# Optimization experiments

Measured on AMD Instinct MI355X. Metric: run time of the kernel, lower is better.

Reference implementation:

```python
import jax, jax.numpy as jnp
import numpy as np
import math

HEAD_DIM = 128
N_HEADS = 32
N_KV_HEADS = 8
ROPE_THETA = 10000.0


def _rotate_half(x):
    x1, x2 = jnp.split(x, 2, axis=-1)
    return jnp.concatenate([-x2, x1], axis=-1)


def _rope_cos_sin(position_ids, head_dim, theta):
    # position_ids: [B, S] int
    inv_freq = 1.0 / (theta ** (jnp.arange(0, head_dim, 2, dtype=jnp.float32) / head_dim))
    freqs = position_ids.astype(jnp.float32)[..., None] * inv_freq[None, None, :]  # [B,S,D/2]
    emb = jnp.concatenate([freqs, freqs], axis=-1)  # [B,S,D]
    return jnp.cos(emb), jnp.sin(emb)


def setup_inputs() -> dict:
    key = jax.random.key(0)
    k1, k2, k3, k4, k5 = jax.random.split(key, 5)
    B, S, H = 1, 2048, 4096
    hidden_states = jax.random.normal(k1, (B, S, H), dtype=jnp.float32)
    Wq = jax.random.normal(k2, (N_HEADS * HEAD_DIM, H), dtype=jnp.float32) * (1.0 / math.sqrt(H))
    Wk = jax.random.normal(k3, (N_KV_HEADS * HEAD_DIM, H), dtype=jnp.float32) * (1.0 / math.sqrt(H))
    Wv = jax.random.normal(k4, (N_KV_HEADS * HEAD_DIM, H), dtype=jnp.float32) * (1.0 / math.sqrt(H))
    Wo = jax.random.normal(k5, (H, N_HEADS * HEAD_DIM), dtype=jnp.float32) * (1.0 / math.sqrt(H))
    position_ids = jnp.arange(S, dtype=jnp.int32)[None, :]
    return {"hidden_states": hidden_states, "Wq": Wq, "Wk": Wk, "Wv": Wv, "Wo": Wo,
            "position_ids": position_ids}


def reference(hidden_states, Wq, Wk, Wv, Wo, position_ids):
    B, S, H = hidden_states.shape
    d = HEAD_DIM
    groups = N_HEADS // N_KV_HEADS

    # projections (torch Linear: x @ W^T)
    q = (hidden_states @ Wq.T).reshape(B, S, N_HEADS, d).transpose(0, 2, 1, 3)      # [B,Hq,S,d]
    k = (hidden_states @ Wk.T).reshape(B, S, N_KV_HEADS, d).transpose(0, 2, 1, 3)   # [B,Hk,S,d]
    v = (hidden_states @ Wv.T).reshape(B, S, N_KV_HEADS, d).transpose(0, 2, 1, 3)

    cos, sin = _rope_cos_sin(position_ids, d, ROPE_THETA)  # [B,S,d]
    cos = cos[:, None, :, :]
    sin = sin[:, None, :, :]
    q = q * cos + _rotate_half(q) * sin
    k = k * cos + _rotate_half(k) * sin

    # GQA: repeat kv heads
    k = jnp.repeat(k, groups, axis=1)  # [B,Hq,S,d]
    v = jnp.repeat(v, groups, axis=1)

    scores = jnp.einsum('bhqd,bhkd->bhqk', q, k) / math.sqrt(d)
    causal = jnp.tril(jnp.ones((S, S), dtype=bool))
    scores = jnp.where(causal[None, None], scores, jnp.finfo(jnp.float32).min)
    attn = jax.nn.softmax(scores.astype(jnp.float32), axis=-1).astype(q.dtype)

    out = jnp.einsum('bhqk,bhkd->bhqd', attn, v)        # [B,Hq,S,d]
    out = out.transpose(0, 2, 1, 3).reshape(B, S, N_HEADS * d)
    return out @ Wo.T
```

## Files before the change

kernel.cpp:

```cpp
#include <hip/hip_runtime.h>
#include <hip/hip_bf16.h>
#include <cstdint>
#include <cstddef>

#define S_LEN 2048
#define HID   4096
#define HD    128
#define NH    32
#define NKV   8
#define KVW   (NKV * HD)
#define QKVN  (HID + 2 * KVW)

typedef __bf16 bf16x8_t __attribute__((ext_vector_type(8)));
typedef float  f32x4_t  __attribute__((ext_vector_type(4)));
typedef unsigned short u16x8_t __attribute__((ext_vector_type(8)));

__device__ __forceinline__ unsigned short f2b(float f) {
  unsigned u = __float_as_uint(f);
  u += 0x7FFFu + ((u >> 16) & 1u);
  return (unsigned short)(u >> 16);
}
__device__ __forceinline__ float b2f(unsigned short v) {
  return __uint_as_float(((unsigned)v) << 16);
}
__device__ __forceinline__ void gld_lds16(const void* g, void* l) {
  __builtin_amdgcn_global_load_lds(
      (const __attribute__((address_space(1))) void*)g,
      (__attribute__((address_space(3))) void*)l, 16, 0, 0);
}

__global__ void cvt_kernel(const float* __restrict__ src,
                           unsigned short* __restrict__ dst, int n4) {
  int i = blockIdx.x * blockDim.x + threadIdx.x;
  int stride = gridDim.x * blockDim.x;
  for (; i < n4; i += stride) {
    float4 v = reinterpret_cast<const float4*>(src)[i];
    ushort4 o;
    o.x = f2b(v.x); o.y = f2b(v.y); o.z = f2b(v.z); o.w = f2b(v.w);
    reinterpret_cast<ushort4*>(dst)[i] = o;
  }
}

__global__ void rope_kernel(unsigned short* __restrict__ Q,
                            unsigned short* __restrict__ Kb,
                            const int* __restrict__ pos_ids) {
  const int total = S_LEN * (NH + NKV) * 64;
  int idx = blockIdx.x * blockDim.x + threadIdx.x;
  int stride = gridDim.x * blockDim.x;
  for (; idx < total; idx += stride) {
    int s   = idx / ((NH + NKV) * 64);
    int rem = idx % ((NH + NKV) * 64);
    int hp  = rem >> 6;
    int i   = rem & 63;
    unsigned short* ptr; int W, h;
    if (hp < NH) { ptr = Q;  W = HID; h = hp; }
    else         { ptr = Kb; W = KVW; h = hp - NH; }
    float pos = (float)pos_ids[s];
    float ang = pos * __expf(-(float)i * 0.14391156516f);
    float sn, cs;
    sincosf(ang, &sn, &cs);
    size_t base = (size_t)s * W + (size_t)h * HD + i;
    float lo = b2f(ptr[base]);
    float hi = b2f(ptr[base + 64]);
    ptr[base]      = f2b(lo * cs - hi * sn);
    ptr[base + 64] = f2b(hi * cs + lo * sn);
  }
}

template <int BN, int MODE>
__global__ __launch_bounds__(512, 2) void gemm8p_kernel(
    const unsigned short* __restrict__ A, const unsigned short* __restrict__ B,
    void* __restrict__ C0, void* __restrict__ C1, void* __restrict__ C2,
    int N, int K) {
  constexpr int NFR = BN / 64;
  constexpr int ABYTES = 256 * 128;
  constexpr int TILE_LDS = ABYTES + BN * 128;
  constexpr int VM_N = NFR + 2;
  __shared__ char ldsB[2 * TILE_LDS];

  const int tid  = threadIdx.x;
  const int lane = tid & 63;
  const int wid  = tid >> 6;
  const int wm = wid >> 2, wn = wid & 3;
  const int lr = lane & 15, g = lane >> 4;
  const int bm = blockIdx.y * 256;
  const int bn = blockIdx.x * BN;
  const int nk = K >> 6;
  const int ni = nk >> 1;
  const int xr = (lr & 7) << 4;

  auto stage_u = [&](int t, int u) {
    if (t >= nk) return;
    const int riu = tid >> 3;
    const int cbs = ((tid & 7) << 4) ^ ((riu & 7) << 4);
    const char* src;
    if (u < 4)
      src = (const char*)A + ((size_t)(bm + u * 64 + riu) * K + t * 64) * 2 + cbs;
    else
      src = (const char*)B + ((size_t)(bn + (u - 4) * 64 + riu) * K + t * 64) * 2 + cbs;
    gld_lds16(src, ldsB + (t & 1) * TILE_LDS + u * 8192 + tid * 16);
  };

  auto rdA = [&](const char* bb, int m, int k) {
    const int row = wm * 128 + m * 16 + lr;
    return *(const bf16x8_t*)(bb + row * 128 + ((k * 64 + g * 16) ^ xr));
  };
  auto rdB = [&](const char* bb, int n, int k) {
    const int row = wn * (BN / 4) + n * 16 + lr;
    return *(const bf16x8_t*)(bb + ABYTES + row * 128 + ((k * 64 + g * 16) ^ xr));
  };

  for (int t = 0; t < 2; ++t)
    for (int u = 0; u < 4 + NFR; ++u) stage_u(t, u);
  asm volatile("s_waitcnt vmcnt(0)" ::: "memory");
  __builtin_amdgcn_sched_barrier(0);
  __builtin_amdgcn_s_barrier();

  f32x4_t acc[8][NFR];
#pragma unroll
  for (int m = 0; m < 8; ++m)
#pragma unroll
    for (int n = 0; n < NFR; ++n) acc[m][n] = f32x4_t{0.f, 0.f, 0.f, 0.f};

  bf16x8_t bfr[NFR][2], af[2][2];

#define MFMA_BLOCK(MB)                                                        \
  __builtin_amdgcn_s_setprio(1);                                              \
  _Pragma("unroll") for (int m = 0; m < 2; ++m)                               \
    _Pragma("unroll") for (int n = 0; n < NFR; ++n)                           \
      _Pragma("unroll") for (int k = 0; k < 2; ++k)                           \
        acc[(MB) + m][n] = __builtin_amdgcn_mfma_f32_16x16x32_bf16(           \
            af[m][k], bfr[n][k], acc[(MB) + m][n], 0, 0, 0);                  \
  __builtin_amdgcn_s_setprio(0);

#define GATE()                                                                \
  __builtin_amdgcn_s_barrier();                                               \
  asm volatile("s_waitcnt lgkmcnt(0)" ::: "memory");                          \
  __builtin_amdgcn_sched_barrier(0);

#define RD_A2(bb, m0)                                                         \
  _Pragma("unroll") for (int m = 0; m < 2; ++m)                               \
    _Pragma("unroll") for (int k = 0; k < 2; ++k)                             \
      af[m][k] = rdA(bb, (m0) + m, k);

  for (int i = 0; i < ni; ++i) {
    const char* baseE = ldsB;
    const char* baseO = ldsB + TILE_LDS;
    const int tO = 2 * i + 1, tE2 = 2 * i + 2, tO2 = 2 * i + 3;
    const bool last = (i == ni - 1);

#pragma unroll
    for (int n = 0; n < NFR; ++n)
#pragma unroll
      for (int k = 0; k < 2; ++k) bfr[n][k] = rdB(baseE, n, k);
    RD_A2(baseE, 0);
    if (i > 0) { stage_u(tO, 1); stage_u(tO, 3); }
    GATE(); MFMA_BLOCK(0);
    __builtin_amdgcn_s_barrier();

    RD_A2(baseE, 2);
    stage_u(tE2, 4); stage_u(tE2, 5);
    GATE(); MFMA_BLOCK(2);
    __builtin_amdgcn_s_barrier();

    RD_A2(baseE, 4);
    if constexpr (NFR == 3) { stage_u(tE2, 6); stage_u(tE2, 0); }
    else                    { stage_u(tE2, 0); stage_u(tE2, 2); }
    GATE(); MFMA_BLOCK(4);
    __builtin_amdgcn_s_barrier();

    RD_A2(baseE, 6);
    if constexpr (NFR == 3) { stage_u(tE2, 2); }
    GATE(); MFMA_BLOCK(6);
    if (last) { asm volatile("s_waitcnt vmcnt(0)" ::: "memory"); }
    else      { asm volatile("s_waitcnt vmcnt(%0)" :: "n"(VM_N) : "memory"); }
    __builtin_amdgcn_sched_barrier(0);
    __builtin_amdgcn_s_barrier();

#pragma unroll
    for (int n = 0; n < NFR; ++n)
#pragma unroll
      for (int k = 0; k < 2; ++k) bfr[n][k] = rdB(baseO, n, k);
    RD_A2(baseO, 0);
    stage_u(tE2, 1); stage_u(tE2, 3);
    GATE(); MFMA_BLOCK(0);
    __builtin_amdgcn_s_barrier();

    RD_A2(baseO, 2);
    stage_u(tO2, 4); stage_u(tO2, 5);
    GATE(); MFMA_BLOCK(2);
    __builtin_amdgcn_s_barrier();

    RD_A2(baseO, 4);
    if constexpr (NFR == 3) { stage_u(tO2, 6); stage_u(tO2, 0); }
    else                    { stage_u(tO2, 0); stage_u(tO2, 2); }
    GATE(); MFMA_BLOCK(4);
    __builtin_amdgcn_s_barrier();

    RD_A2(baseO, 6);
    if constexpr (NFR == 3) { stage_u(tO2, 2); }
    GATE(); MFMA_BLOCK(6);
    if (!last) { asm volatile("s_waitcnt vmcnt(%0)" :: "n"(VM_N) : "memory"); }
    __builtin_amdgcn_sched_barrier(0);
    __builtin_amdgcn_s_barrier();
  }
#undef MFMA_BLOCK
#undef GATE
#undef RD_A2

#pragma unroll
  for (int mf = 0; mf < 8; ++mf) {
    const int row0 = bm + wm * 128 + mf * 16 + g * 4;
#pragma unroll
    for (int nf = 0; nf < NFR; ++nf) {
      const int col = bn + wn * (BN / 4) + nf * 16 + lr;
      if constexpr (MODE == 1) {
#pragma unroll
        for (int r = 0; r < 4; ++r)
          ((float*)C0)[(size_t)(row0 + r) * N + col] = acc[mf][nf][r];
      } else {
        if (col < HID) {
#pragma unroll
          for (int r = 0; r < 4; ++r)
            ((unsigned short*)C0)[(size_t)(row0 + r) * HID + col] = f2b(acc[mf][nf][r]);
        } else if (col < HID + KVW) {
#pragma unroll
          for (int r = 0; r < 4; ++r)
            ((unsigned short*)C1)[(size_t)(row0 + r) * KVW + (col - HID)] = f2b(acc[mf][nf][r]);
        } else {
          const int c2 = col - HID - KVW;
          ushort4 w;
          w.x = f2b(acc[mf][nf][0]); w.y = f2b(acc[mf][nf][1]);
          w.z = f2b(acc[mf][nf][2]); w.w = f2b(acc[mf][nf][3]);
          *(ushort4*)(void*)&((unsigned short*)C2)[(size_t)c2 * S_LEN + row0] = w;
        }
      }
    }
  }
}

__global__ __launch_bounds__(256) void attn_kernel(
    const unsigned short* __restrict__ Q, const unsigned short* __restrict__ K,
    const unsigned short* __restrict__ VtG, unsigned short* __restrict__ O) {
  __shared__ unsigned short Kl[64][136];
  __shared__ unsigned short Vt[128][72];
  __shared__ unsigned short Pl[4][16][72];

  const int tid  = threadIdx.x;
  const int lane = tid & 63;
  const int wave = tid >> 6;
  const int h    = blockIdx.y;
  const int kvh  = h >> 2;
  const int pair = blockIdx.x;
  const int lr   = lane & 15;
  const int g    = lane >> 4;
  const int lk8  = g * 8;
  const float scale = 0.08838834764831845f;
  const unsigned short* Vbase = VtG + (size_t)kvh * HD * S_LEN;

  const int ksr = tid >> 4, ksc = (tid & 15) * 8;
  const int vsr = tid >> 3, vsc = (tid & 7) * 8;

  for (int pass = 0; pass < 2; ++pass) {
    const int qb = pass == 0 ? (31 - pair) : pair;
    const int q0 = qb * 64;
    const int qrow = q0 + wave * 16;
    const int nkv = qb + 1;

    bf16x8_t qf[4];
    {
      const unsigned short* qp = Q + (size_t)(qrow + lr) * HID + (size_t)h * HD;
#pragma unroll
      for (int c = 0; c < 4; ++c)
        qf[c] = *(const bf16x8_t*)(const void*)(qp + c * 32 + lk8);
    }
    f32x4_t oacc[8];
#pragma unroll
    for (int c = 0; c < 8; ++c) oacc[c] = f32x4_t{0.f, 0.f, 0.f, 0.f};
    float m_run = -3e38f, l_run = 0.f;

    u16x8_t kr[4], vr[4];
#pragma unroll
    for (int i = 0; i < 4; ++i)
      kr[i] = *(const u16x8_t*)(const void*)(K + (size_t)(ksr + i * 16) * KVW +
                                             (size_t)kvh * HD + ksc);
#pragma unroll
    for (int i = 0; i < 4; ++i)
      vr[i] = *(const u16x8_t*)(const void*)(Vbase + (size_t)(vsr + i * 32) * S_LEN + vsc);

    for (int it = 0; it < nkv; ++it) {
      const int kv0 = it * 64;
      __builtin_amdgcn_s_barrier();
#pragma unroll
      for (int i = 0; i < 4; ++i)
        *(u16x8_t*)(void*)&Kl[ksr + i * 16][ksc] = kr[i];
#pragma unroll
      for (int i = 0; i < 4; ++i)
        *(u16x8_t*)(void*)&Vt[vsr + i * 32][vsc] = vr[i];
      if (it + 1 < nkv) {
        const int kn = kv0 + 64;
#pragma unroll
        for (int i = 0; i < 4; ++i)
          kr[i] = *(const u16x8_t*)(const void*)(K + (size_t)(kn + ksr + i * 16) * KVW +
                                                 (size_t)kvh * HD + ksc);
#pragma unroll
        for (int i = 0; i < 4; ++i)
          vr[i] = *(const u16x8_t*)(const void*)(Vbase + (size_t)(vsr + i * 32) * S_LEN +
                                                 kn + vsc);
      }
      asm volatile("s_waitcnt lgkmcnt(0)" ::: "memory");
      __builtin_amdgcn_sched_barrier(0);
      __builtin_amdgcn_s_barrier();

      f32x4_t sacc[4];
#pragma unroll
      for (int n = 0; n < 4; ++n) sacc[n] = f32x4_t{0.f, 0.f, 0.f, 0.f};
#pragma unroll
      for (int c = 0; c < 4; ++c) {
        bf16x8_t qc = qf[c];
#pragma unroll
        for (int n = 0; n < 4; ++n) {
          bf16x8_t kf = *(const bf16x8_t*)(const void*)&Kl[n * 16 + lr][c * 32 + lk8];
          sacc[n] = __builtin_amdgcn_mfma_f32_16x16x32_bf16(kf, qc, sacc[n], 0, 0, 0);
        }
      }

      const int qg = qrow + lr;
      const bool diag = (it == nkv - 1);
      float p[16];
      float mloc = -3e38f;
#pragma unroll
      for (int n = 0; n < 4; ++n)
#pragma unroll
        for (int r = 0; r < 4; ++r) {
          float x = sacc[n][r] * scale;
          if (diag) {
            int kg = kv0 + n * 16 + g * 4 + r;
            if (kg > qg) x = -3e38f;
          }
          p[n * 4 + r] = x;
          mloc = fmaxf(mloc, x);
        }
      mloc = fmaxf(mloc, __shfl_xor(mloc, 16));
      mloc = fmaxf(mloc, __shfl_xor(mloc, 32));

      if (__any(mloc > m_run + 8.f)) {
        float m_new = fmaxf(m_run, mloc);
        float alpha = __expf(m_run - m_new);
        float a4[4];
#pragma unroll
        for (int r = 0; r < 4; ++r) a4[r] = __shfl(alpha, g * 4 + r);
#pragma unroll
        for (int c = 0; c < 8; ++c)
#pragma unroll
          for (int r = 0; r < 4; ++r) oacc[c][r] *= a4[r];
        l_run *= alpha;
        m_run = m_new;
      }

      float ssum = 0.f;
#pragma unroll
      for (int i = 0; i < 16; ++i) {
        float e = __expf(p[i] - m_run);
        p[i] = e;
        ssum += e;
      }
      ssum += __shfl_xor(ssum, 16);
      ssum += __shfl_xor(ssum, 32);
      l_run += ssum;

#pragma unroll
      for (int n = 0; n < 4; ++n) {
        ushort4 w;
        w.x = f2b(p[n * 4 + 0]); w.y = f2b(p[n * 4 + 1]);
        w.z = f2b(p[n * 4 + 2]); w.w = f2b(p[n * 4 + 3]);
        *(ushort4*)(void*)&Pl[wave][lr][n * 16 + g * 4] = w;
      }

#pragma unroll
      for (int half = 0; half < 2; ++half) {
        bf16x8_t pf = *(const bf16x8_t*)(const void*)&Pl[wave][lr][half * 32 + lk8];
#pragma unroll
        for (int c = 0; c < 8; ++c) {
          bf16x8_t vf = *(const bf16x8_t*)(const void*)&Vt[c * 16 + lr][half * 32 + lk8];
          oacc[c] = __builtin_amdgcn_mfma_f32_16x16x32_bf16(pf, vf, oacc[c], 0, 0, 0);
        }
      }
    }

    float linv[4];
#pragma unroll
    for (int r = 0; r < 4; ++r) linv[r] = 1.f / __shfl(l_run, g * 4 + r);
#pragma unroll
    for (int r = 0; r < 4; ++r) {
      int row = qrow + g * 4 + r;
#pragma unroll
      for (int c = 0; c < 8; ++c)
        O[(size_t)row * HID + (size_t)h * HD + c * 16 + lr] = f2b(oacc[c][r] * linv[r]);
    }
  }
}

extern "C" void kernel_launch(void* const* d_in, const int* in_sizes, int n_in,
                              void* d_out, int out_size, void* d_ws, size_t ws_size,
                              hipStream_t stream) {
  (void)in_sizes; (void)n_in; (void)out_size; (void)ws_size;
  const float* X  = (const float*)d_in[0];
  const float* Wq = (const float*)d_in[1];
  const float* Wk = (const float*)d_in[2];
  const float* Wv = (const float*)d_in[3];
  const float* Wo = (const float*)d_in[4];
  const int*  pos = (const int*)d_in[5];
  float* out = (float*)d_out;

  unsigned short* Xb  = (unsigned short*)d_ws;
  unsigned short* Wqb = Xb  + (size_t)S_LEN * HID;
  unsigned short* Wkb = Wqb + (size_t)HID * HID;
  unsigned short* Wvb = Wkb + (size_t)KVW * HID;
  unsigned short* Wob = Wvb + (size_t)KVW * HID;
  unsigned short* Qb  = Wob + (size_t)HID * HID;
  unsigned short* Kb  = Qb  + (size_t)S_LEN * HID;
  unsigned short* VtB = Kb  + (size_t)S_LEN * KVW;
  unsigned short* AOb = VtB + (size_t)S_LEN * KVW;

  auto cvt = [&](const float* s, unsigned short* d, size_t n) {
    int n4 = (int)(n / 4);
    int grid = (n4 + 255) / 256;
    if (grid > 4096) grid = 4096;
    cvt_kernel<<<grid, 256, 0, stream>>>(s, d, n4);
  };
  cvt(X,  Xb,  (size_t)S_LEN * HID);
  cvt(Wq, Wqb, (size_t)HID * HID);
  cvt(Wk, Wkb, (size_t)KVW * HID);
  cvt(Wv, Wvb, (size_t)KVW * HID);
  cvt(Wo, Wob, (size_t)HID * HID);

  gemm8p_kernel<192, 2><<<dim3(QKVN / 192, S_LEN / 256), 512, 0, stream>>>(
      Xb, Wqb, Qb, Kb, VtB, QKVN, HID);

  rope_kernel<<<2048, 256, 0, stream>>>(Qb, Kb, pos);

  attn_kernel<<<dim3(16, NH), 256, 0, stream>>>(Qb, Kb, VtB, AOb);

  gemm8p_kernel<128, 1><<<dim3(HID / 128, S_LEN / 256), 512, 0, stream>>>(
      AOb, Wob, out, nullptr, nullptr, HID, HID);
}
```

Measured before the change: 308.1 us.

## Halve GEMM M-tile to 128 rows and restructure pipeline for more blocks

Both projection GEMMs now use a 128-row M tile instead of 256 rows. The staging schedule, accumulator count, LDS footprint and wait counts are restructured to match, with four MFMA phases per K-pair instead of eight, and launch bounds are raised to 4 blocks per CU. The grids get twice as many blocks, which is meant to fill the 256 CUs better (the QKV grid was 32x8 and the output grid 32x8). In exchange, arithmetic intensity per tile drops and B-tile reuse is halved, so global and L2 traffic increases.

```diff
diff --git a/kernel.cpp b/kernel.cpp
--- a/kernel.cpp
+++ b/kernel.cpp
@@ -68,14 +68,13 @@
 }
 
 template <int BN, int MODE>
-__global__ __launch_bounds__(512, 2) void gemm8p_kernel(
+__global__ __launch_bounds__(512, 4) void gemm4p_kernel(
     const unsigned short* __restrict__ A, const unsigned short* __restrict__ B,
     void* __restrict__ C0, void* __restrict__ C1, void* __restrict__ C2,
     int N, int K) {
   constexpr int NFR = BN / 64;
-  constexpr int ABYTES = 256 * 128;
+  constexpr int ABYTES = 128 * 128;
   constexpr int TILE_LDS = ABYTES + BN * 128;
-  constexpr int VM_N = NFR + 2;
   __shared__ char ldsB[2 * TILE_LDS];
 
   const int tid  = threadIdx.x;
@@ -83,7 +82,7 @@
   const int wid  = tid >> 6;
   const int wm = wid >> 2, wn = wid & 3;
   const int lr = lane & 15, g = lane >> 4;
-  const int bm = blockIdx.y * 256;
+  const int bm = blockIdx.y * 128;
   const int bn = blockIdx.x * BN;
   const int nk = K >> 6;
   const int ni = nk >> 1;
@@ -94,15 +93,15 @@
     const int riu = tid >> 3;
     const int cbs = ((tid & 7) << 4) ^ ((riu & 7) << 4);
     const char* src;
-    if (u < 4)
+    if (u < 2)
       src = (const char*)A + ((size_t)(bm + u * 64 + riu) * K + t * 64) * 2 + cbs;
     else
-      src = (const char*)B + ((size_t)(bn + (u - 4) * 64 + riu) * K + t * 64) * 2 + cbs;
+      src = (const char*)B + ((size_t)(bn + (u - 2) * 64 + riu) * K + t * 64) * 2 + cbs;
     gld_lds16(src, ldsB + (t & 1) * TILE_LDS + u * 8192 + tid * 16);
   };
 
   auto rdA = [&](const char* bb, int m, int k) {
-    const int row = wm * 128 + m * 16 + lr;
+    const int row = wm * 64 + m * 16 + lr;
     return *(const bf16x8_t*)(bb + row * 128 + ((k * 64 + g * 16) ^ xr));
   };
   auto rdB = [&](const char* bb, int n, int k) {
@@ -111,14 +110,14 @@
   };
 
   for (int t = 0; t < 2; ++t)
-    for (int u = 0; u < 4 + NFR; ++u) stage_u(t, u);
+    for (int u = 0; u < 2 + NFR; ++u) stage_u(t, u);
   asm volatile("s_waitcnt vmcnt(0)" ::: "memory");
   __builtin_amdgcn_sched_barrier(0);
   __builtin_amdgcn_s_barrier();
 
-  f32x4_t acc[8][NFR];
-#pragma unroll
-  for (int m = 0; m < 8; ++m)
+  f32x4_t acc[4][NFR];
+#pragma unroll
+  for (int m = 0; m < 4; ++m)
 #pragma unroll
     for (int n = 0; n < NFR; ++n) acc[m][n] = f32x4_t{0.f, 0.f, 0.f, 0.f};
 
@@ -143,74 +142,54 @@
     _Pragma("unroll") for (int k = 0; k < 2; ++k)                             \
       af[m][k] = rdA(bb, (m0) + m, k);
 
+#define RD_B(bb)                                                              \
+  _Pragma("unroll") for (int n = 0; n < NFR; ++n)                             \
+    _Pragma("unroll") for (int k = 0; k < 2; ++k)                             \
+      bfr[n][k] = rdB(bb, n, k);
+
   for (int i = 0; i < ni; ++i) {
-    const char* baseE = ldsB;
-    const char* baseO = ldsB + TILE_LDS;
+    const char* bE = ldsB;
+    const char* bO = ldsB + TILE_LDS;
     const int tO = 2 * i + 1, tE2 = 2 * i + 2, tO2 = 2 * i + 3;
     const bool last = (i == ni - 1);
 
-#pragma unroll
-    for (int n = 0; n < NFR; ++n)
-#pragma unroll
-      for (int k = 0; k < 2; ++k) bfr[n][k] = rdB(baseE, n, k);
-    RD_A2(baseE, 0);
-    if (i > 0) { stage_u(tO, 1); stage_u(tO, 3); }
+    RD_B(bE);
+    RD_A2(bE, 0);
+    if (i > 0) { stage_u(tO, 0); stage_u(tO, 1); }
     GATE(); MFMA_BLOCK(0);
     __builtin_amdgcn_s_barrier();
 
-    RD_A2(baseE, 2);
-    stage_u(tE2, 4); stage_u(tE2, 5);
+    RD_A2(bE, 2);
+#pragma unroll
+    for (int u = 0; u < NFR; ++u) stage_u(tE2, 2 + u);
     GATE(); MFMA_BLOCK(2);
-    __builtin_amdgcn_s_barrier();
-
-    RD_A2(baseE, 4);
-    if constexpr (NFR == 3) { stage_u(tE2, 6); stage_u(tE2, 0); }
-    else                    { stage_u(tE2, 0); stage_u(tE2, 2); }
-    GATE(); MFMA_BLOCK(4);
-    __builtin_amdgcn_s_barrier();
-
-    RD_A2(baseE, 6);
-    if constexpr (NFR == 3) { stage_u(tE2, 2); }
-    GATE(); MFMA_BLOCK(6);
     if (last) { asm volatile("s_waitcnt vmcnt(0)" ::: "memory"); }
-    else      { asm volatile("s_waitcnt vmcnt(%0)" :: "n"(VM_N) : "memory"); }
+    else      { asm volatile("s_waitcnt vmcnt(%0)" :: "n"(NFR) : "memory"); }
     __builtin_amdgcn_sched_barrier(0);
     __builtin_amdgcn_s_barrier();
 
-#pragma unroll
-    for (int n = 0; n < NFR; ++n)
-#pragma unroll
-      for (int k = 0; k < 2; ++k) bfr[n][k] = rdB(baseO, n, k);
-    RD_A2(baseO, 0);
-    stage_u(tE2, 1); stage_u(tE2, 3);
+    RD_B(bO);
+    RD_A2(bO, 0);
+    stage_u(tE2, 0); stage_u(tE2, 1);
     GATE(); MFMA_BLOCK(0);
     __builtin_amdgcn_s_barrier();
 
-    RD_A2(baseO, 2);
-    stage_u(tO2, 4); stage_u(tO2, 5);
+    RD_A2(bO, 2);
+#pragma unroll
+    for (int u = 0; u < NFR; ++u) stage_u(tO2, 2 + u);
     GATE(); MFMA_BLOCK(2);
-    __builtin_amdgcn_s_barrier();
-
-    RD_A2(baseO, 4);
-    if constexpr (NFR == 3) { stage_u(tO2, 6); stage_u(tO2, 0); }
-    else                    { stage_u(tO2, 0); stage_u(tO2, 2); }
-    GATE(); MFMA_BLOCK(4);
-    __builtin_amdgcn_s_barrier();
-
-    RD_A2(baseO, 6);
-    if constexpr (NFR == 3) { stage_u(tO2, 2); }
-    GATE(); MFMA_BLOCK(6);
-    if (!last) { asm volatile("s_waitcnt vmcnt(%0)" :: "n"(VM_N) : "memory"); }
+    if (!last) { asm volatile("s_waitcnt vmcnt(%0)" :: "n"(NFR) : "memory"); }
     __builtin_amdgcn_sched_barrier(0);
     __builtin_amdgcn_s_barrier();
   }
 #undef MFMA_BLOCK
 #undef GATE
 #undef RD_A2
-
-#pragma unroll
-  for (int mf = 0; mf < 8; ++mf) {
-    const int row0 = bm + wm * 128 + mf * 16 + g * 4;
+#undef RD_B
+
+#pragma unroll
+  for (int mf = 0; mf < 4; ++mf) {
+    const int row0 = bm + wm * 64 + mf * 16 + g * 4;
 #pragma unroll
     for (int nf = 0; nf < NFR; ++nf) {
       const int col = bn + wn * (BN / 4) + nf * 16 + lr;
@@ -435,13 +414,13 @@
   cvt(Wv, Wvb, (size_t)KVW * HID);
   cvt(Wo, Wob, (size_t)HID * HID);
 
-  gemm8p_kernel<192, 2><<<dim3(QKVN / 192, S_LEN / 256), 512, 0, stream>>>(
+  gemm4p_kernel<192, 2><<<dim3(QKVN / 192, S_LEN / 128), 512, 0, stream>>>(
       Xb, Wqb, Qb, Kb, VtB, QKVN, HID);
 
   rope_kernel<<<2048, 256, 0, stream>>>(Qb, Kb, pos);
 
   attn_kernel<<<dim3(16, NH), 256, 0, stream>>>(Qb, Kb, VtB, AOb);
 
-  gemm8p_kernel<128, 1><<<dim3(HID / 128, S_LEN / 256), 512, 0, stream>>>(
+  gemm4p_kernel<128, 1><<<dim3(HID / 128, S_LEN / 128), 512, 0, stream>>>(
       AOb, Wob, out, nullptr, nullptr, HID, HID);
 }
```

Result: faster. 299.2 us (-2.9%).
